# Kernel tuning notes

Measured on AMD Instinct MI355X. Metric: run time of the kernel, lower is better.

The kernel has to match this reference:

```python
import jax, jax.numpy as jnp
import numpy as np

N_NODES = 100000
N_EDGES = 1600000
IN_CH, HID_CH, LAT = 32, 32, 16


def _gcn_layer(h, W, b, src, dst, norm):
    # PyG GCNConv: h' = scatter_add(norm * (h W)[src] -> dst) + b
    h = h @ W                                   # [N, out]
    msg = h[src] * norm[:, None]                # [E+N, out] gather
    out = jax.ops.segment_sum(msg, dst, num_segments=N_NODES)
    return out + b


def setup_inputs() -> dict:
    key = jax.random.key(0)
    ks = jax.random.split(key, 8)
    x = jax.random.normal(ks[0], (N_NODES, IN_CH), dtype=jnp.float32)
    edge_index = jax.random.randint(ks[1], (2, N_EDGES), 0, N_NODES, dtype=jnp.int32)
    def glorot(k, fan_in, fan_out):
        lim = np.sqrt(6.0 / (fan_in + fan_out)).astype(np.float32)
        return jax.random.uniform(k, (fan_in, fan_out), jnp.float32, -lim, lim)
    return {
        "x": x,
        "edge_index": edge_index,
        "W1": glorot(ks[2], IN_CH, HID_CH),
        "b1": jnp.zeros((HID_CH,), jnp.float32),
        "Wmu": glorot(ks[3], HID_CH, LAT),
        "bmu": jnp.zeros((LAT,), jnp.float32),
        "Wlv": glorot(ks[4], HID_CH, LAT),
        "blv": jnp.zeros((LAT,), jnp.float32),
    }


def reference(x, edge_index, W1, b1, Wmu, bmu, Wlv, blv):
    # Add self-loops (GCNConv default add_self_loops=True)
    loops = jnp.arange(N_NODES, dtype=edge_index.dtype)
    src = jnp.concatenate([edge_index[0], loops])
    dst = jnp.concatenate([edge_index[1], loops])
    # Symmetric normalization: deg over destinations, norm = d^-1/2[src] * d^-1/2[dst]
    deg = jax.ops.segment_sum(jnp.ones_like(dst, dtype=x.dtype), dst,
                              num_segments=N_NODES)
    dinv = jnp.where(deg > 0, jax.lax.rsqrt(deg), 0.0)
    norm = dinv[src] * dinv[dst]                # [E+N]

    h = jax.nn.relu(_gcn_layer(x, W1, b1, src, dst, norm))
    mu = _gcn_layer(h, Wmu, bmu, src, dst, norm)
    logvar = _gcn_layer(h, Wlv, blv, src, dst, norm)
    return (mu, logvar)
```

## Files before the change

### kernel.cpp

```cpp
#include <hip/hip_runtime.h>
#include <hip/hip_fp16.h>

#define N_NODES 100000
#define N_EDGES 1600000
#define NCB 98
#define CAPC 17500
#define P1_CHUNK 2048
#define P1_BLOCKS 782
#define BK 64
#define NBF 1563
#define CAPF 1408
#define P2_SPLIT 8

__global__ __launch_bounds__(1024) void k_binit(int* __restrict__ cursor1,
                                                int* __restrict__ cursor2) {
    int i = blockIdx.x * 1024 + threadIdx.x;
    if (i < NCB) cursor1[i] = i * CAPC;
    if (i < NBF) cursor2[i] = i * CAPF;
}

__global__ __launch_bounds__(256) void k_part1(const int* __restrict__ src,
                                               const int* __restrict__ dst,
                                               int* __restrict__ cursor1,
                                               unsigned* __restrict__ packed1) {
    __shared__ int bh[NCB];
    __shared__ int base[NCB];
    int t = threadIdx.x;
    if (t < NCB) bh[t] = 0;
    __syncthreads();
    int e0 = blockIdx.x * P1_CHUNK;
    int e1 = e0 + P1_CHUNK; if (e1 > N_EDGES) e1 = N_EDGES;
    for (int e = e0 + t; e < e1; e += 256)
        atomicAdd(&bh[((unsigned)dst[e]) >> 10], 1);
    __syncthreads();
    if (t < NCB) {
        int c = bh[t];
        base[t] = (c > 0) ? atomicAdd(&cursor1[t], c) : 0;
        bh[t] = 0;
    }
    __syncthreads();
    for (int e = e0 + t; e < e1; e += 256) {
        unsigned d = (unsigned)dst[e];
        int b = d >> 10;
        int r = atomicAdd(&bh[b], 1);
        int pos = base[b] + r;
        if (pos < (b + 1) * CAPC)
            packed1[pos] = ((d & 1023u) << 17) | (unsigned)src[e];
    }
}

__global__ __launch_bounds__(256) void k_part2(const unsigned* __restrict__ packed1,
                                               const int* __restrict__ cursor1,
                                               int* __restrict__ cursor2,
                                               unsigned* __restrict__ packed2) {
    __shared__ int bh[16];
    __shared__ int base[16];
    int t = threadIdx.x;
    int c = blockIdx.x / P2_SPLIT;
    int k = blockIdx.x % P2_SPLIT;
    int cc = cursor1[c] - c * CAPC; if (cc > CAPC) cc = CAPC;
    int s0 = c * CAPC + (k * cc) / P2_SPLIT;
    int s1 = c * CAPC + ((k + 1) * cc) / P2_SPLIT;
    if (t < 16) bh[t] = 0;
    __syncthreads();
    for (int i = s0 + t; i < s1; i += 256)
        atomicAdd(&bh[(packed1[i] >> 17) >> 6], 1);
    __syncthreads();
    if (t < 16) {
        int cnt = bh[t];
        int fb = c * 16 + t;
        base[t] = (cnt > 0) ? atomicAdd(&cursor2[fb], cnt) : 0;
        bh[t] = 0;
    }
    __syncthreads();
    for (int i = s0 + t; i < s1; i += 256) {
        unsigned pk = packed1[i];
        unsigned dl = pk >> 17;
        int f = dl >> 6;
        int r = atomicAdd(&bh[f], 1);
        int pos = base[f] + r;
        int fb = c * 16 + f;
        if (pos < (fb + 1) * CAPF)
            packed2[pos] = ((dl & 63u) << 17) | (pk & 0x1FFFFu);
    }
}

__global__ __launch_bounds__(256) void k_csrx(const unsigned* __restrict__ packed2,
                                              const int* __restrict__ cursor2,
                                              const float* __restrict__ x,
                                              const float* __restrict__ W1,
                                              int* __restrict__ rowBeg,
                                              int* __restrict__ rowEnd,
                                              float* __restrict__ dinv,
                                              int* __restrict__ srcSorted,
                                              __half* __restrict__ p1) {
    __shared__ int cnt[BK];
    __shared__ int s[BK];
    __shared__ int cur[BK];
    __shared__ float sW[32 * 32];
    int t = threadIdx.x;
    int b = blockIdx.x;
    int seg0 = b * CAPF;
    int cc = cursor2[b] - seg0; if (cc > CAPF) cc = CAPF;
    int segEnd = seg0 + cc;
    if (t < BK) cnt[t] = 0;
    for (int i = t; i < 1024; i += 256) sW[i] = W1[i];
    __syncthreads();
    for (int i = seg0 + t; i < segEnd; i += 256)
        atomicAdd(&cnt[packed2[i] >> 17], 1);
    __syncthreads();
    int v = (t < BK) ? cnt[t] : 0;
    if (t < BK) s[t] = v;
    __syncthreads();
    for (int off = 1; off < BK; off <<= 1) {
        int u = (t < BK && t >= off) ? s[t - off] : 0;
        __syncthreads();
        if (t < BK) s[t] += u;
        __syncthreads();
    }
    int node = b * BK + t;
    if (t < BK) {
        int start = seg0 + s[t] - v;
        if (node < N_NODES) {
            rowBeg[node] = start;
            rowEnd[node] = start + v;
            dinv[node] = rsqrtf((float)(v + 1));
        }
        cur[t] = start;
    }
    __syncthreads();
    for (int i = seg0 + t; i < segEnd; i += 256) {
        unsigned pk = packed2[i];
        int pos = atomicAdd(&cur[pk >> 17], 1);
        srcSorted[pos] = (int)(pk & 0x1FFFFu);
    }
    int lane = t & 31;
    for (int r = (t >> 5); r < BK; r += 8) {
        int nd = b * BK + r;
        if (nd >= N_NODES) break;
        float xv = x[nd * 32 + lane];
        float a = 0.f;
#pragma unroll
        for (int k = 0; k < 32; ++k) {
            float xk = __shfl(xv, k, 32);
            a += xk * sW[k * 32 + lane];
        }
        float di = rsqrtf((float)(cnt[r] + 1));
        p1[nd * 32 + lane] = __float2half(di * a);
    }
}

__device__ __forceinline__ void acc4(float2 v, float& c0, float& c1, float& c2, float& c3) {
    __half2 lo = *reinterpret_cast<__half2*>(&v.x);
    __half2 hi = *reinterpret_cast<__half2*>(&v.y);
    c0 += __low2float(lo); c1 += __high2float(lo);
    c2 += __low2float(hi); c3 += __high2float(hi);
}

__device__ __forceinline__ void gatherRow8(const int* __restrict__ srcSorted,
                                           const float2* __restrict__ P,
                                           int beg, int end, int l,
                                           float& r0, float& r1, float& r2, float& r3) {
    float a0 = 0.f, a1 = 0.f, a2 = 0.f, a3 = 0.f;
    float b0 = 0.f, b1 = 0.f, b2 = 0.f, b3 = 0.f;
    int base = beg;
    for (; base + 16 <= end; base += 16) {
        int sA = srcSorted[base + l];
        int sB = srcSorted[base + 8 + l];
        float2 v0 = P[__shfl(sA, 0, 8) * 8 + l];
        float2 v1 = P[__shfl(sA, 1, 8) * 8 + l];
        float2 v2 = P[__shfl(sA, 2, 8) * 8 + l];
        float2 v3 = P[__shfl(sA, 3, 8) * 8 + l];
        float2 v4 = P[__shfl(sA, 4, 8) * 8 + l];
        float2 v5 = P[__shfl(sA, 5, 8) * 8 + l];
        float2 v6 = P[__shfl(sA, 6, 8) * 8 + l];
        float2 v7 = P[__shfl(sA, 7, 8) * 8 + l];
        float2 w0 = P[__shfl(sB, 0, 8) * 8 + l];
        float2 w1 = P[__shfl(sB, 1, 8) * 8 + l];
        float2 w2 = P[__shfl(sB, 2, 8) * 8 + l];
        float2 w3 = P[__shfl(sB, 3, 8) * 8 + l];
        float2 w4 = P[__shfl(sB, 4, 8) * 8 + l];
        float2 w5 = P[__shfl(sB, 5, 8) * 8 + l];
        float2 w6 = P[__shfl(sB, 6, 8) * 8 + l];
        float2 w7 = P[__shfl(sB, 7, 8) * 8 + l];
        acc4(v0, a0, a1, a2, a3); acc4(v1, b0, b1, b2, b3);
        acc4(v2, a0, a1, a2, a3); acc4(v3, b0, b1, b2, b3);
        acc4(v4, a0, a1, a2, a3); acc4(v5, b0, b1, b2, b3);
        acc4(v6, a0, a1, a2, a3); acc4(v7, b0, b1, b2, b3);
        acc4(w0, a0, a1, a2, a3); acc4(w1, b0, b1, b2, b3);
        acc4(w2, a0, a1, a2, a3); acc4(w3, b0, b1, b2, b3);
        acc4(w4, a0, a1, a2, a3); acc4(w5, b0, b1, b2, b3);
        acc4(w6, a0, a1, a2, a3); acc4(w7, b0, b1, b2, b3);
    }
    if (base + 8 <= end) {
        int sA = srcSorted[base + l];
        float2 v0 = P[__shfl(sA, 0, 8) * 8 + l];
        float2 v1 = P[__shfl(sA, 1, 8) * 8 + l];
        float2 v2 = P[__shfl(sA, 2, 8) * 8 + l];
        float2 v3 = P[__shfl(sA, 3, 8) * 8 + l];
        float2 v4 = P[__shfl(sA, 4, 8) * 8 + l];
        float2 v5 = P[__shfl(sA, 5, 8) * 8 + l];
        float2 v6 = P[__shfl(sA, 6, 8) * 8 + l];
        float2 v7 = P[__shfl(sA, 7, 8) * 8 + l];
        acc4(v0, a0, a1, a2, a3); acc4(v1, b0, b1, b2, b3);
        acc4(v2, a0, a1, a2, a3); acc4(v3, b0, b1, b2, b3);
        acc4(v4, a0, a1, a2, a3); acc4(v5, b0, b1, b2, b3);
        acc4(v6, a0, a1, a2, a3); acc4(v7, b0, b1, b2, b3);
        base += 8;
    }
    if (base < end) {
        int idx = base + l;
        int myS = (idx < end) ? srcSorted[idx] : 0;
        int n = end - base;
        for (int j = 0; j < n; ++j) {
            int sx = __shfl(myS, j, 8);
            float2 v = P[sx * 8 + l];
            acc4(v, a0, a1, a2, a3);
        }
    }
    r0 = a0 + b0; r1 = a1 + b1; r2 = a2 + b2; r3 = a3 + b3;
}

__global__ __launch_bounds__(256) void k_gx2(const int* __restrict__ rowBeg,
                                             const int* __restrict__ rowEnd,
                                             const int* __restrict__ srcSorted,
                                             const __half* __restrict__ p1,
                                             const float* __restrict__ dinv,
                                             const float* __restrict__ b1,
                                             const float* __restrict__ Wmu,
                                             const float* __restrict__ Wlv,
                                             __half* __restrict__ p2) {
    __shared__ float sW[32 * 32];
    __shared__ float sB[32];
    int t = threadIdx.x;
    for (int i = t; i < 1024; i += 256) {
        int k = i >> 5, oc = i & 31;
        sW[i] = (oc < 16) ? Wmu[k * 16 + oc] : Wlv[k * 16 + (oc - 16)];
    }
    if (t < 32) sB[t] = b1[t];
    __syncthreads();
    int l = t & 7;
    int node = blockIdx.x * 32 + (t >> 3);
    const float2* P = (const float2*)p1;
    float g0, g1, g2, g3;
    gatherRow8(srcSorted, P, rowBeg[node], rowEnd[node], l, g0, g1, g2, g3);
    float di = dinv[node];
    float s0, s1, s2, s3;
    {
        float2 ps = P[node * 8 + l];
        __half2 lo = *reinterpret_cast<__half2*>(&ps.x);
        __half2 hi = *reinterpret_cast<__half2*>(&ps.y);
        s0 = __low2float(lo); s1 = __high2float(lo);
        s2 = __low2float(hi); s3 = __high2float(hi);
    }
    float h0 = fmaxf(di * (g0 + s0) + sB[4 * l + 0], 0.f);
    float h1 = fmaxf(di * (g1 + s1) + sB[4 * l + 1], 0.f);
    float h2 = fmaxf(di * (g2 + s2) + sB[4 * l + 2], 0.f);
    float h3 = fmaxf(di * (g3 + s3) + sB[4 * l + 3], 0.f);
    float o0 = 0.f, o1 = 0.f, o2 = 0.f, o3 = 0.f;
    const float4* W4 = (const float4*)sW;
#pragma unroll
    for (int m = 0; m < 8; ++m) {
        float ha = __shfl(h0, m, 8);
        float hb = __shfl(h1, m, 8);
        float hc = __shfl(h2, m, 8);
        float hd = __shfl(h3, m, 8);
        float4 wa = W4[(4 * m + 0) * 8 + l];
        float4 wb = W4[(4 * m + 1) * 8 + l];
        float4 wc = W4[(4 * m + 2) * 8 + l];
        float4 wd = W4[(4 * m + 3) * 8 + l];
        o0 += ha * wa.x + hb * wb.x + hc * wc.x + hd * wd.x;
        o1 += ha * wa.y + hb * wb.y + hc * wc.y + hd * wd.y;
        o2 += ha * wa.z + hb * wb.z + hc * wc.z + hd * wd.z;
        o3 += ha * wa.w + hb * wb.w + hc * wc.w + hd * wd.w;
    }
    __half2 lo = __floats2half2_rn(di * o0, di * o1);
    __half2 hi = __floats2half2_rn(di * o2, di * o3);
    float2 st;
    st.x = *reinterpret_cast<float*>(&lo);
    st.y = *reinterpret_cast<float*>(&hi);
    ((float2*)p2)[node * 8 + l] = st;
}

__global__ __launch_bounds__(256) void k_gfin(const int* __restrict__ rowBeg,
                                              const int* __restrict__ rowEnd,
                                              const int* __restrict__ srcSorted,
                                              const __half* __restrict__ p2,
                                              const float* __restrict__ dinv,
                                              const float* __restrict__ bmu,
                                              const float* __restrict__ blv,
                                              float* __restrict__ out) {
    __shared__ float sB[32];
    int t = threadIdx.x;
    if (t < 32) sB[t] = (t < 16) ? bmu[t] : blv[t - 16];
    __syncthreads();
    int l = t & 7;
    int node = blockIdx.x * 32 + (t >> 3);
    const float2* P = (const float2*)p2;
    float g0, g1, g2, g3;
    gatherRow8(srcSorted, P, rowBeg[node], rowEnd[node], l, g0, g1, g2, g3);
    float di = dinv[node];
    float s0, s1, s2, s3;
    {
        float2 ps = P[node * 8 + l];
        __half2 lo = *reinterpret_cast<__half2*>(&ps.x);
        __half2 hi = *reinterpret_cast<__half2*>(&ps.y);
        s0 = __low2float(lo); s1 = __high2float(lo);
        s2 = __low2float(hi); s3 = __high2float(hi);
    }
    float4 v;
    v.x = di * (g0 + s0) + sB[4 * l + 0];
    v.y = di * (g1 + s1) + sB[4 * l + 1];
    v.z = di * (g2 + s2) + sB[4 * l + 2];
    v.w = di * (g3 + s3) + sB[4 * l + 3];
    if (l < 4) {
        ((float4*)out)[node * 4 + l] = v;
    } else {
        ((float4*)(out + (size_t)N_NODES * 16))[node * 4 + (l - 4)] = v;
    }
}

extern "C" void kernel_launch(void* const* d_in, const int* in_sizes, int n_in,
                              void* d_out, int out_size, void* d_ws, size_t ws_size,
                              hipStream_t stream) {
    const float* x   = (const float*)d_in[0];
    const int*   ei  = (const int*)d_in[1];
    const float* W1  = (const float*)d_in[2];
    const float* b1  = (const float*)d_in[3];
    const float* Wmu = (const float*)d_in[4];
    const float* bmu = (const float*)d_in[5];
    const float* Wlv = (const float*)d_in[6];
    const float* blv = (const float*)d_in[7];
    float* out = (float*)d_out;

    const int* src = ei;
    const int* dst = ei + N_EDGES;

    int* cursor1      = (int*)d_ws;
    int* cursor2      = cursor1 + NCB;
    int* rowBeg       = cursor2 + NBF;
    int* rowEnd       = rowBeg + N_NODES;
    float* dinv       = (float*)(rowEnd + N_NODES);
    unsigned* packed1 = (unsigned*)(dinv + N_NODES);
    unsigned* packed2 = packed1 + (size_t)NCB * CAPC;
    int* srcSorted    = (int*)(packed2 + (size_t)NBF * CAPF);
    __half* p1h       = (__half*)packed1;
    __half* p2h       = (__half*)packed2;

    const int gBlocks = N_NODES / 32;

    k_binit<<<2, 1024, 0, stream>>>(cursor1, cursor2);
    k_part1<<<P1_BLOCKS, 256, 0, stream>>>(src, dst, cursor1, packed1);
    k_part2<<<NCB * P2_SPLIT, 256, 0, stream>>>(packed1, cursor1, cursor2, packed2);
    k_csrx <<<NBF, 256, 0, stream>>>(packed2, cursor2, x, W1,
                                     rowBeg, rowEnd, dinv, srcSorted, p1h);
    k_gx2  <<<gBlocks, 256, 0, stream>>>(rowBeg, rowEnd, srcSorted, p1h, dinv,
                                         b1, Wmu, Wlv, p2h);
    k_gfin <<<gBlocks, 256, 0, stream>>>(rowBeg, rowEnd, srcSorted, p2h, dinv,
                                         bmu, blv, out);
}
```

Before: 207.9 us.

## Gather with 4 lanes per node using 16-byte loads and half2 partial sums

Each node row is now gathered by 4 lanes issuing 16-byte float4 loads instead of 8 lanes issuing 8-byte loads. Neighbour contributions are summed in half precision in groups of eight before being converted to float. A zero padding row at index N_NODES replaces the tail loops, so the inner loop is branch-free. The second transform is restructured to match, workspace buffers are aligned, and the partition split is doubled. These changes aim for fewer, wider memory transactions and fewer instructions per gathered edge, at the cost of some precision from the half-precision partial sums.

```diff
diff --git a/kernel.cpp b/kernel.cpp
--- a/kernel.cpp
+++ b/kernel.cpp
@@ -10,7 +10,7 @@
 #define BK 64
 #define NBF 1563
 #define CAPF 1408
-#define P2_SPLIT 8
+#define P2_SPLIT 16
 
 __global__ __launch_bounds__(1024) void k_binit(int* __restrict__ cursor1,
                                                 int* __restrict__ cursor2) {
@@ -137,7 +137,11 @@
     int lane = t & 31;
     for (int r = (t >> 5); r < BK; r += 8) {
         int nd = b * BK + r;
-        if (nd >= N_NODES) break;
+        if (nd > N_NODES) break;
+        if (nd == N_NODES) {
+            p1[nd * 32 + lane] = __float2half(0.f);
+            continue;
+        }
         float xv = x[nd * 32 + lane];
         float a = 0.f;
 #pragma unroll
@@ -150,75 +154,38 @@
     }
 }
 
-__device__ __forceinline__ void acc4(float2 v, float& c0, float& c1, float& c2, float& c3) {
-    __half2 lo = *reinterpret_cast<__half2*>(&v.x);
-    __half2 hi = *reinterpret_cast<__half2*>(&v.y);
-    c0 += __low2float(lo); c1 += __high2float(lo);
-    c2 += __low2float(hi); c3 += __high2float(hi);
-}
-
-__device__ __forceinline__ void gatherRow8(const int* __restrict__ srcSorted,
-                                           const float2* __restrict__ P,
+__device__ __forceinline__ __half2 h2of(const float4& v, int c) {
+    return reinterpret_cast<const __half2*>(&v)[c];
+}
+
+__device__ __forceinline__ void gatherRow4(const int* __restrict__ srcSorted,
+                                           const float4* __restrict__ P,
                                            int beg, int end, int l,
-                                           float& r0, float& r1, float& r2, float& r3) {
-    float a0 = 0.f, a1 = 0.f, a2 = 0.f, a3 = 0.f;
-    float b0 = 0.f, b1 = 0.f, b2 = 0.f, b3 = 0.f;
-    int base = beg;
-    for (; base + 16 <= end; base += 16) {
-        int sA = srcSorted[base + l];
-        int sB = srcSorted[base + 8 + l];
-        float2 v0 = P[__shfl(sA, 0, 8) * 8 + l];
-        float2 v1 = P[__shfl(sA, 1, 8) * 8 + l];
-        float2 v2 = P[__shfl(sA, 2, 8) * 8 + l];
-        float2 v3 = P[__shfl(sA, 3, 8) * 8 + l];
-        float2 v4 = P[__shfl(sA, 4, 8) * 8 + l];
-        float2 v5 = P[__shfl(sA, 5, 8) * 8 + l];
-        float2 v6 = P[__shfl(sA, 6, 8) * 8 + l];
-        float2 v7 = P[__shfl(sA, 7, 8) * 8 + l];
-        float2 w0 = P[__shfl(sB, 0, 8) * 8 + l];
-        float2 w1 = P[__shfl(sB, 1, 8) * 8 + l];
-        float2 w2 = P[__shfl(sB, 2, 8) * 8 + l];
-        float2 w3 = P[__shfl(sB, 3, 8) * 8 + l];
-        float2 w4 = P[__shfl(sB, 4, 8) * 8 + l];
-        float2 w5 = P[__shfl(sB, 5, 8) * 8 + l];
-        float2 w6 = P[__shfl(sB, 6, 8) * 8 + l];
-        float2 w7 = P[__shfl(sB, 7, 8) * 8 + l];
-        acc4(v0, a0, a1, a2, a3); acc4(v1, b0, b1, b2, b3);
-        acc4(v2, a0, a1, a2, a3); acc4(v3, b0, b1, b2, b3);
-        acc4(v4, a0, a1, a2, a3); acc4(v5, b0, b1, b2, b3);
-        acc4(v6, a0, a1, a2, a3); acc4(v7, b0, b1, b2, b3);
-        acc4(w0, a0, a1, a2, a3); acc4(w1, b0, b1, b2, b3);
-        acc4(w2, a0, a1, a2, a3); acc4(w3, b0, b1, b2, b3);
-        acc4(w4, a0, a1, a2, a3); acc4(w5, b0, b1, b2, b3);
-        acc4(w6, a0, a1, a2, a3); acc4(w7, b0, b1, b2, b3);
-    }
-    if (base + 8 <= end) {
-        int sA = srcSorted[base + l];
-        float2 v0 = P[__shfl(sA, 0, 8) * 8 + l];
-        float2 v1 = P[__shfl(sA, 1, 8) * 8 + l];
-        float2 v2 = P[__shfl(sA, 2, 8) * 8 + l];
-        float2 v3 = P[__shfl(sA, 3, 8) * 8 + l];
-        float2 v4 = P[__shfl(sA, 4, 8) * 8 + l];
-        float2 v5 = P[__shfl(sA, 5, 8) * 8 + l];
-        float2 v6 = P[__shfl(sA, 6, 8) * 8 + l];
-        float2 v7 = P[__shfl(sA, 7, 8) * 8 + l];
-        acc4(v0, a0, a1, a2, a3); acc4(v1, b0, b1, b2, b3);
-        acc4(v2, a0, a1, a2, a3); acc4(v3, b0, b1, b2, b3);
-        acc4(v4, a0, a1, a2, a3); acc4(v5, b0, b1, b2, b3);
-        acc4(v6, a0, a1, a2, a3); acc4(v7, b0, b1, b2, b3);
-        base += 8;
-    }
-    if (base < end) {
-        int idx = base + l;
-        int myS = (idx < end) ? srcSorted[idx] : 0;
-        int n = end - base;
-        for (int j = 0; j < n; ++j) {
-            int sx = __shfl(myS, j, 8);
-            float2 v = P[sx * 8 + l];
-            acc4(v, a0, a1, a2, a3);
-        }
-    }
-    r0 = a0 + b0; r1 = a1 + b1; r2 = a2 + b2; r3 = a3 + b3;
+                                           float* __restrict__ acc ) {
+    for (int base = beg; base < end; base += 8) {
+        int i0 = base + l, i1 = base + 4 + l;
+        int sA = (i0 < end) ? srcSorted[i0] : N_NODES;
+        int sB = (i1 < end) ? srcSorted[i1] : N_NODES;
+        float4 v0 = P[__shfl(sA, 0, 4) * 4 + l];
+        float4 v1 = P[__shfl(sA, 1, 4) * 4 + l];
+        float4 v2 = P[__shfl(sA, 2, 4) * 4 + l];
+        float4 v3 = P[__shfl(sA, 3, 4) * 4 + l];
+        float4 v4 = P[__shfl(sB, 0, 4) * 4 + l];
+        float4 v5 = P[__shfl(sB, 1, 4) * 4 + l];
+        float4 v6 = P[__shfl(sB, 2, 4) * 4 + l];
+        float4 v7 = P[__shfl(sB, 3, 4) * 4 + l];
+#pragma unroll
+        for (int c = 0; c < 4; ++c) {
+            __half2 s01 = __hadd2(h2of(v0, c), h2of(v1, c));
+            __half2 s23 = __hadd2(h2of(v2, c), h2of(v3, c));
+            __half2 s45 = __hadd2(h2of(v4, c), h2of(v5, c));
+            __half2 s67 = __hadd2(h2of(v6, c), h2of(v7, c));
+            __half2 sum = __hadd2(__hadd2(s01, s23), __hadd2(s45, s67));
+            float2 f = __half22float2(sum);
+            acc[2 * c]     += f.x;
+            acc[2 * c + 1] += f.y;
+        }
+    }
 }
 
 __global__ __launch_bounds__(256) void k_gx2(const int* __restrict__ rowBeg,
@@ -239,47 +206,49 @@
     }
     if (t < 32) sB[t] = b1[t];
     __syncthreads();
-    int l = t & 7;
-    int node = blockIdx.x * 32 + (t >> 3);
-    const float2* P = (const float2*)p1;
-    float g0, g1, g2, g3;
-    gatherRow8(srcSorted, P, rowBeg[node], rowEnd[node], l, g0, g1, g2, g3);
+    int l = t & 3;
+    int node = blockIdx.x * 64 + (t >> 2);
+    if (node > N_NODES) return;
+    const float4* P = (const float4*)p1;
+    if (node == N_NODES) {
+        ((float4*)p2)[node * 4 + l] = make_float4(0.f, 0.f, 0.f, 0.f);
+        return;
+    }
+    float acc[8] = {0.f, 0.f, 0.f, 0.f, 0.f, 0.f, 0.f, 0.f};
+    gatherRow4(srcSorted, P, rowBeg[node], rowEnd[node], l, acc);
     float di = dinv[node];
-    float s0, s1, s2, s3;
-    {
-        float2 ps = P[node * 8 + l];
-        __half2 lo = *reinterpret_cast<__half2*>(&ps.x);
-        __half2 hi = *reinterpret_cast<__half2*>(&ps.y);
-        s0 = __low2float(lo); s1 = __high2float(lo);
-        s2 = __low2float(hi); s3 = __high2float(hi);
-    }
-    float h0 = fmaxf(di * (g0 + s0) + sB[4 * l + 0], 0.f);
-    float h1 = fmaxf(di * (g1 + s1) + sB[4 * l + 1], 0.f);
-    float h2 = fmaxf(di * (g2 + s2) + sB[4 * l + 2], 0.f);
-    float h3 = fmaxf(di * (g3 + s3) + sB[4 * l + 3], 0.f);
-    float o0 = 0.f, o1 = 0.f, o2 = 0.f, o3 = 0.f;
+    float4 ps = P[node * 4 + l];
+    float h[8];
+#pragma unroll
+    for (int c = 0; c < 4; ++c) {
+        float2 f = __half22float2(h2of(ps, c));
+        h[2 * c]     = fmaxf(di * (acc[2 * c]     + f.x) + sB[8 * l + 2 * c],     0.f);
+        h[2 * c + 1] = fmaxf(di * (acc[2 * c + 1] + f.y) + sB[8 * l + 2 * c + 1], 0.f);
+    }
+    float o[8] = {0.f, 0.f, 0.f, 0.f, 0.f, 0.f, 0.f, 0.f};
     const float4* W4 = (const float4*)sW;
 #pragma unroll
-    for (int m = 0; m < 8; ++m) {
-        float ha = __shfl(h0, m, 8);
-        float hb = __shfl(h1, m, 8);
-        float hc = __shfl(h2, m, 8);
-        float hd = __shfl(h3, m, 8);
-        float4 wa = W4[(4 * m + 0) * 8 + l];
-        float4 wb = W4[(4 * m + 1) * 8 + l];
-        float4 wc = W4[(4 * m + 2) * 8 + l];
-        float4 wd = W4[(4 * m + 3) * 8 + l];
-        o0 += ha * wa.x + hb * wb.x + hc * wc.x + hd * wd.x;
-        o1 += ha * wa.y + hb * wb.y + hc * wc.y + hd * wd.y;
-        o2 += ha * wa.z + hb * wb.z + hc * wc.z + hd * wd.z;
-        o3 += ha * wa.w + hb * wb.w + hc * wc.w + hd * wd.w;
-    }
-    __half2 lo = __floats2half2_rn(di * o0, di * o1);
-    __half2 hi = __floats2half2_rn(di * o2, di * o3);
-    float2 st;
-    st.x = *reinterpret_cast<float*>(&lo);
-    st.y = *reinterpret_cast<float*>(&hi);
-    ((float2*)p2)[node * 8 + l] = st;
+    for (int m = 0; m < 4; ++m) {
+#pragma unroll
+        for (int j = 0; j < 8; ++j) {
+            float hk = __shfl(h[j], m, 4);
+            int k = 8 * m + j;
+            float4 wa = W4[k * 8 + 2 * l];
+            float4 wb = W4[k * 8 + 2 * l + 1];
+            o[0] += hk * wa.x; o[1] += hk * wa.y; o[2] += hk * wa.z; o[3] += hk * wa.w;
+            o[4] += hk * wb.x; o[5] += hk * wb.y; o[6] += hk * wb.z; o[7] += hk * wb.w;
+        }
+    }
+    __half2 r0 = __floats2half2_rn(di * o[0], di * o[1]);
+    __half2 r1 = __floats2half2_rn(di * o[2], di * o[3]);
+    __half2 r2 = __floats2half2_rn(di * o[4], di * o[5]);
+    __half2 r3 = __floats2half2_rn(di * o[6], di * o[7]);
+    float4 st;
+    st.x = *reinterpret_cast<float*>(&r0);
+    st.y = *reinterpret_cast<float*>(&r1);
+    st.z = *reinterpret_cast<float*>(&r2);
+    st.w = *reinterpret_cast<float*>(&r3);
+    ((float4*)p2)[node * 4 + l] = st;
 }
 
 __global__ __launch_bounds__(256) void k_gfin(const int* __restrict__ rowBeg,
@@ -294,30 +263,28 @@
     int t = threadIdx.x;
     if (t < 32) sB[t] = (t < 16) ? bmu[t] : blv[t - 16];
     __syncthreads();
-    int l = t & 7;
-    int node = blockIdx.x * 32 + (t >> 3);
-    const float2* P = (const float2*)p2;
-    float g0, g1, g2, g3;
-    gatherRow8(srcSorted, P, rowBeg[node], rowEnd[node], l, g0, g1, g2, g3);
+    int l = t & 3;
+    int node = blockIdx.x * 64 + (t >> 2);
+    if (node >= N_NODES) return;
+    const float4* P = (const float4*)p2;
+    float acc[8] = {0.f, 0.f, 0.f, 0.f, 0.f, 0.f, 0.f, 0.f};
+    gatherRow4(srcSorted, P, rowBeg[node], rowEnd[node], l, acc);
     float di = dinv[node];
-    float s0, s1, s2, s3;
-    {
-        float2 ps = P[node * 8 + l];
-        __half2 lo = *reinterpret_cast<__half2*>(&ps.x);
-        __half2 hi = *reinterpret_cast<__half2*>(&ps.y);
-        s0 = __low2float(lo); s1 = __high2float(lo);
-        s2 = __low2float(hi); s3 = __high2float(hi);
-    }
-    float4 v;
-    v.x = di * (g0 + s0) + sB[4 * l + 0];
-    v.y = di * (g1 + s1) + sB[4 * l + 1];
-    v.z = di * (g2 + s2) + sB[4 * l + 2];
-    v.w = di * (g3 + s3) + sB[4 * l + 3];
-    if (l < 4) {
-        ((float4*)out)[node * 4 + l] = v;
-    } else {
-        ((float4*)(out + (size_t)N_NODES * 16))[node * 4 + (l - 4)] = v;
-    }
+    float4 ps = P[node * 4 + l];
+    float v[8];
+#pragma unroll
+    for (int c = 0; c < 4; ++c) {
+        float2 f = __half22float2(h2of(ps, c));
+        v[2 * c]     = di * (acc[2 * c]     + f.x) + sB[8 * l + 2 * c];
+        v[2 * c + 1] = di * (acc[2 * c + 1] + f.y) + sB[8 * l + 2 * c + 1];
+    }
+    float4 o0 = make_float4(v[0], v[1], v[2], v[3]);
+    float4 o1 = make_float4(v[4], v[5], v[6], v[7]);
+    float4* dst = (l < 2) ? (float4*)out
+                          : (float4*)(out + (size_t)N_NODES * 16);
+    int base = node * 4 + (l & 1) * 2;
+    dst[base]     = o0;
+    dst[base + 1] = o1;
 }
 
 extern "C" void kernel_launch(void* const* d_in, const int* in_sizes, int n_in,
@@ -336,18 +303,22 @@
     const int* src = ei;
     const int* dst = ei + N_EDGES;
 
-    int* cursor1      = (int*)d_ws;
-    int* cursor2      = cursor1 + NCB;
-    int* rowBeg       = cursor2 + NBF;
-    int* rowEnd       = rowBeg + N_NODES;
-    float* dinv       = (float*)(rowEnd + N_NODES);
-    unsigned* packed1 = (unsigned*)(dinv + N_NODES);
-    unsigned* packed2 = packed1 + (size_t)NCB * CAPC;
-    int* srcSorted    = (int*)(packed2 + (size_t)NBF * CAPF);
+    size_t off = 0;
+    int* cursor1 = (int*)d_ws;                          off += NCB;
+    int* cursor2 = (int*)d_ws + off;                    off += NBF;
+    int* rowBeg  = (int*)d_ws + off;                    off += N_NODES;
+    int* rowEnd  = (int*)d_ws + off;                    off += N_NODES;
+    float* dinv  = (float*)((int*)d_ws + off);          off += N_NODES;
+    off = (off + 63) & ~(size_t)63;
+    unsigned* packed1 = (unsigned*)((int*)d_ws + off);  off += (size_t)NCB * CAPC;
+    off = (off + 63) & ~(size_t)63;
+    unsigned* packed2 = (unsigned*)((int*)d_ws + off);  off += (size_t)NBF * CAPF;
+    off = (off + 63) & ~(size_t)63;
+    int* srcSorted    = (int*)d_ws + off;
     __half* p1h       = (__half*)packed1;
     __half* p2h       = (__half*)packed2;
 
-    const int gBlocks = N_NODES / 32;
+    const int gBlocks = 1563;
 
     k_binit<<<2, 1024, 0, stream>>>(cursor1, cursor2);
     k_part1<<<P1_BLOCKS, 256, 0, stream>>>(src, dst, cursor1, packed1);
```

Result: faster. 195.4 us (-6.0%).
